# Optimization experiments

Hardware: AMD Instinct MI355X
Metric: run time of the kernel (lower is better)

The kernel has to match this reference:

```python
import jax, jax.numpy as jnp
import numpy as np
from jax import lax

B, T, K = 4096, 512, 7


def setup_inputs() -> dict:
    key = jax.random.key(0)
    k1, k2, k3, k4, k5, k6 = jax.random.split(key, 6)
    emissions = jax.random.normal(k1, (B, T, K), dtype=jnp.float32)
    # variable-length sequences: mask is a contiguous prefix of ones (token_ids.gt(0))
    lengths = jax.random.randint(k2, (B,), T // 2, T + 1)
    mask = (jnp.arange(T)[None, :] < lengths[:, None]).astype(jnp.int32)
    tags = jax.random.randint(k3, (B, T), 0, K).astype(jnp.int64)
    transitions = jax.random.normal(k4, (K, K), dtype=jnp.float32) * 0.1
    start_transitions = jax.random.normal(k5, (K,), dtype=jnp.float32) * 0.1
    end_transitions = jax.random.normal(k6, (K,), dtype=jnp.float32) * 0.1
    return {
        "emissions": emissions,
        "mask": mask,
        "tags": tags,
        "transitions": transitions,
        "start_transitions": start_transitions,
        "end_transitions": end_transitions,
    }


def _crf_nll(emissions, mask, tags, transitions, start_transitions, end_transitions):
    maskf = mask.astype(emissions.dtype)  # [B, T]
    # ---- numerator: score of the gold path ----
    em_tag = jnp.take_along_axis(emissions, tags[..., None], axis=2)[..., 0]  # [B, T]
    score = start_transitions[tags[:, 0]] + em_tag[:, 0]  # [B]
    trans_score = transitions[tags[:, :-1], tags[:, 1:]]  # [B, T-1]
    score = score + jnp.sum((trans_score + em_tag[:, 1:]) * maskf[:, 1:], axis=1)
    last_idx = jnp.sum(mask, axis=1).astype(jnp.int32) - 1  # [B]
    last_tag = jnp.take_along_axis(tags, last_idx[:, None].astype(tags.dtype), axis=1)[:, 0]
    score = score + end_transitions[last_tag]
    # ---- denominator: log partition via forward algorithm (stable logsumexp DP) ----
    alpha0 = start_transitions[None, :] + emissions[:, 0]  # [B, K]

    def step(alpha, xs):
        em_t, m_t = xs  # [B, K], [B]
        # alpha[b, i] + transitions[i, j] + em_t[b, j] -> logsumexp over i
        nxt = jax.nn.logsumexp(alpha[:, :, None] + transitions[None, :, :] + em_t[:, None, :], axis=1)
        alpha = jnp.where(m_t[:, None] > 0, nxt, alpha)
        return alpha, None

    xs = (jnp.swapaxes(emissions[:, 1:], 0, 1), jnp.swapaxes(mask[:, 1:], 0, 1))  # [T-1, B, K], [T-1, B]
    alpha, _ = lax.scan(step, alpha0, xs)
    log_z = jax.nn.logsumexp(alpha + end_transitions[None, :], axis=1)  # [B]
    return jnp.mean(log_z - score)


def reference(emissions, mask, tags, transitions, start_transitions, end_transitions):
    return _crf_nll(emissions, mask, tags, transitions, start_transitions, end_transitions)
```

## Files before the change

### kernel.cpp

```cpp
#include <hip/hip_runtime.h>

#define BB 4096
#define TT 512
#define KK 7
#define SS 16
#define NMAT (BB * 31 * 7)

__device__ __forceinline__ float fexp2(float x){ float r; asm("v_exp_f32 %0, %1" : "=v"(r) : "v"(x)); return r; }
__device__ __forceinline__ float flog2(float x){ float r; asm("v_log_f32 %0, %1" : "=v"(r) : "v"(x)); return r; }
__device__ __forceinline__ float uni(float x){ return __int_as_float(__builtin_amdgcn_readfirstlane(__float_as_int(x))); }

__global__ __launch_bounds__(256) void crf_p1(
    const float* __restrict__ em, const int* __restrict__ msk,
    const float* __restrict__ trn, const float* __restrict__ stt,
    float* __restrict__ wsA, float* __restrict__ wsP)
{
  const float L2E = 1.44269504088896340736f;
  int tid = blockIdx.x * 256 + threadIdx.x;

  float e2[49];
  #pragma unroll
  for (int i = 0; i < 49; i++) e2[i] = uni(fexp2(trn[i] * L2E));

  if (tid < NMAT) {
    int q = tid / 7, i = tid - q * 7;
    int b = q / 31, c = q - b * 31 + 1;
    int t0 = c * SS;
    const size_t eb = (size_t)b * (TT * KK);

    float R[KK];
    #pragma unroll
    for (int j = 0; j < KK; j++) R[j] = (j == i) ? 1.f : 0.f;
    float Lr = 0.f; int cnt = 0; int alive = 1;

    for (int g = 0; g < 4; g++) {
      if (!alive) break;
      int t = t0 + 4 * g;
      float em_[28];
      #pragma unroll
      for (int p = 0; p < 7; p++) {
        float4 f = *(const float4*)(em + eb + (size_t)t * KK + 4 * p);
        em_[4*p+0] = f.x; em_[4*p+1] = f.y; em_[4*p+2] = f.z; em_[4*p+3] = f.w;
      }
      int4 m4 = *(const int4*)(msk + b * TT + t);
      int ms[4] = {m4.x, m4.y, m4.z, m4.w};
      #pragma unroll
      for (int s = 0; s < 4; s++) {
        if (!ms[s]) { alive = 0; break; }
        cnt++;
        float acc[KK];
        #pragma unroll
        for (int j = 0; j < KK; j++) acc[j] = R[0] * e2[j];
        #pragma unroll
        for (int k = 1; k < KK; k++)
          #pragma unroll
          for (int j = 0; j < KK; j++) acc[j] = fmaf(R[k], e2[k*KK + j], acc[j]);
        #pragma unroll
        for (int j = 0; j < KK; j++) R[j] = acc[j] * fexp2(em_[s*KK + j] * L2E);
        if ((cnt & 3) == 0) {
          float mm = R[0];
          #pragma unroll
          for (int j = 1; j < KK; j++) mm = fmaxf(mm, R[j]);
          int ex = (int)((__float_as_uint(mm) >> 23) & 255) - 127;
          float scl = __uint_as_float((unsigned)(127 - ex) << 23);
          Lr += (float)ex;
          #pragma unroll
          for (int j = 0; j < KK; j++) R[j] *= scl;
        }
      }
    }
    if (cnt > 0) {
      float* P = wsP + ((size_t)(c - 1) * BB + b) * 49 + i * KK;
      #pragma unroll
      for (int j = 0; j < KK; j++) P[j] = Lr + flog2(R[j]);
    }
  } else {
    int b = tid - NMAT;
    const size_t eb = (size_t)b * (TT * KK);
    float em_[28];
    #pragma unroll
    for (int p = 0; p < 7; p++) {
      float4 f = *(const float4*)(em + eb + 4 * p);
      em_[4*p+0] = f.x; em_[4*p+1] = f.y; em_[4*p+2] = f.z; em_[4*p+3] = f.w;
    }
    int4 m4 = *(const int4*)(msk + b * TT);
    int ms[4] = {m4.x, m4.y, m4.z, m4.w};

    float u[KK], Ls;
    {
      float a2[KK];
      #pragma unroll
      for (int j = 0; j < KK; j++) a2[j] = (stt[j] + em_[j]) * L2E;
      float m = a2[0];
      #pragma unroll
      for (int j = 1; j < KK; j++) m = fmaxf(m, a2[j]);
      #pragma unroll
      for (int j = 0; j < KK; j++) u[j] = fexp2(a2[j] - m);
      Ls = m;
    }
    int cnt = ms[0]; int alive = 1;

    for (int g = 0; g < 4; g++) {
      if (g > 0) {
        if (!alive) break;
        int t = 4 * g;
        #pragma unroll
        for (int p = 0; p < 7; p++) {
          float4 f = *(const float4*)(em + eb + (size_t)t * KK + 4 * p);
          em_[4*p+0] = f.x; em_[4*p+1] = f.y; em_[4*p+2] = f.z; em_[4*p+3] = f.w;
        }
        int4 n4 = *(const int4*)(msk + b * TT + t);
        ms[0] = n4.x; ms[1] = n4.y; ms[2] = n4.z; ms[3] = n4.w;
      }
      #pragma unroll
      for (int s = 0; s < 4; s++) {
        if (g == 0 && s == 0) continue;
        if (!ms[s]) { alive = 0; break; }
        cnt++;
        float acc[KK];
        #pragma unroll
        for (int j = 0; j < KK; j++) acc[j] = u[0] * e2[j];
        #pragma unroll
        for (int k = 1; k < KK; k++)
          #pragma unroll
          for (int j = 0; j < KK; j++) acc[j] = fmaf(u[k], e2[k*KK + j], acc[j]);
        #pragma unroll
        for (int j = 0; j < KK; j++) u[j] = acc[j] * fexp2(em_[s*KK + j] * L2E);
        if ((cnt & 3) == 0) {
          float mm = u[0];
          #pragma unroll
          for (int j = 1; j < KK; j++) mm = fmaxf(mm, u[j]);
          int ex = (int)((__float_as_uint(mm) >> 23) & 255) - 127;
          float scl = __uint_as_float((unsigned)(127 - ex) << 23);
          Ls += (float)ex;
          #pragma unroll
          for (int j = 0; j < KK; j++) u[j] *= scl;
        }
      }
    }
    #pragma unroll
    for (int j = 0; j < KK; j++) wsA[b * 8 + j] = Ls + flog2(u[j]);
  }
}

__global__ __launch_bounds__(256) void crf_p2(
    const float* __restrict__ em, const int* __restrict__ msk,
    const int* __restrict__ tgs, const float* __restrict__ trn,
    const float* __restrict__ stt, const float* __restrict__ ent,
    const float* __restrict__ wsA, const float* __restrict__ wsP,
    float* __restrict__ out)
{
  const float L2E = 1.44269504088896340736f;
  const float LN2 = 0.69314718055994530942f;
  __shared__ float sm[4];
  int w = threadIdx.x >> 6, lane = threadIdx.x & 63;
  int b = blockIdx.x * 4 + w;
  const int* mrow = msk + b * TT;
  const int* trow = tgs + b * TT;
  const size_t eb = (size_t)b * (TT * KK);

  int4 ma = *(const int4*)(mrow + lane * 8);
  int4 mb = *(const int4*)(mrow + lane * 8 + 4);
  int len = ma.x + ma.y + ma.z + ma.w + mb.x + mb.y + mb.z + mb.w;
  #pragma unroll
  for (int o = 1; o < 64; o <<= 1) len += __shfl_xor(len, o);

  int4 ta = *(const int4*)(trow + lane * 8);
  int4 tb = *(const int4*)(trow + lane * 8 + 4);
  int tga[8] = {ta.x, ta.y, ta.z, ta.w, tb.x, tb.y, tb.z, tb.w};
  int tprev = lane ? trow[lane * 8 - 1] : 0;
  float scp = 0.f;
  #pragma unroll
  for (int s = 0; s < 8; s++) {
    int t = lane * 8 + s; int tg = tga[s];
    if (t == 0)          scp += stt[tg] + em[eb + tg];
    else if (t < len)    scp += trn[tprev * KK + tg] + em[eb + (size_t)t * KK + tg];
    if (t == len - 1)    scp += ent[tg];
    tprev = tg;
  }
  float score = scp;
  #pragma unroll
  for (int o = 1; o < 64; o <<= 1) score += __shfl_xor(score, o);

  float A = (lane < KK) ? wsA[b * 8 + lane] : -1e30f;
  int j = (lane < KK) ? lane : 0;
  int nact = (len - 1) >> 4; if (nact > 31) nact = 31;
  const float* Pb = wsP + (size_t)b * 49;
  const size_t cs = (size_t)BB * 49;
  float cur[KK];
  if (nact >= 1) {
    #pragma unroll
    for (int i = 0; i < KK; i++) cur[i] = Pb[i * KK + j];
  }
  for (int c2 = 1; c2 <= nact; c2++) {
    float nxt[KK];
    if (c2 < nact) {
      #pragma unroll
      for (int i = 0; i < KK; i++) nxt[i] = Pb[(size_t)c2 * cs + i * KK + j];
    }
    float v[KK];
    #pragma unroll
    for (int i = 0; i < KK; i++) v[i] = __shfl(A, i) + cur[i];
    float m = v[0];
    #pragma unroll
    for (int i = 1; i < KK; i++) m = fmaxf(m, v[i]);
    float ssum = 0.f;
    #pragma unroll
    for (int i = 0; i < KK; i++) ssum += fexp2(v[i] - m);
    A = m + flog2(ssum);
    #pragma unroll
    for (int i = 0; i < KK; i++) cur[i] = nxt[i];
  }

  float x = (lane < KK) ? A + ent[lane] * L2E : -1e30f;
  float mx = x;
  #pragma unroll
  for (int o = 1; o < 8; o <<= 1) mx = fmaxf(mx, __shfl_xor(mx, o));
  float se = fexp2(x - mx);
  #pragma unroll
  for (int o = 1; o < 8; o <<= 1) se += __shfl_xor(se, o);

  if (lane == 0) {
    float logz = LN2 * (mx + flog2(se));
    sm[w] = (logz - score) * (1.0f / BB);
  }
  __syncthreads();
  if (threadIdx.x == 0) atomicAdd(out, sm[0] + sm[1] + sm[2] + sm[3]);
}

extern "C" void kernel_launch(void* const* d_in, const int* in_sizes, int n_in,
                              void* d_out, int out_size, void* d_ws, size_t ws_size,
                              hipStream_t stream) {
  const float* em  = (const float*)d_in[0];
  const int*   msk = (const int*)d_in[1];
  const int*   tgs = (const int*)d_in[2];
  const float* trn = (const float*)d_in[3];
  const float* stt = (const float*)d_in[4];
  const float* ent = (const float*)d_in[5];
  float* out = (float*)d_out;

  float* wsA = (float*)d_ws;
  float* wsP = wsA + (size_t)BB * 8;

  hipMemsetAsync(out, 0, sizeof(float), stream);
  hipLaunchKernelGGL(crf_p1, dim3((NMAT + BB) / 256), dim3(256), 0, stream,
                     em, msk, trn, stt, wsA, wsP);
  hipLaunchKernelGGL(crf_p2, dim3(BB / 4), dim3(256), 0, stream,
                     em, msk, tgs, trn, stt, ent, wsA, wsP, out);
}
```

Measured before the change: 179.7 us.

## Precompute sequence lengths and exp transitions in a prepass; double-buffer emission loads

Adds a small prepass kernel that computes each sequence's length from the mask and the exponentiated transition matrix once. The chunk kernel then reads the length instead of per-step mask loads, skips fully masked chunks up front, and double-buffers emission loads so the next group is fetched while the current one is computed. Thread-to-chunk mapping is changed so consecutive threads cover different batch rows within the same chunk. The cost is an extra kernel launch and extra workspace, plus a change in memory access pattern.

```diff
diff --git a/kernel.cpp b/kernel.cpp
--- a/kernel.cpp
+++ b/kernel.cpp
@@ -10,9 +10,64 @@
 __device__ __forceinline__ float flog2(float x){ float r; asm("v_log_f32 %0, %1" : "=v"(r) : "v"(x)); return r; }
 __device__ __forceinline__ float uni(float x){ return __int_as_float(__builtin_amdgcn_readfirstlane(__float_as_int(x))); }
 
+__global__ __launch_bounds__(256) void crf_len(
+    const int* __restrict__ msk, const float* __restrict__ trn,
+    int* __restrict__ wlen, float* __restrict__ wse2)
+{
+  const float L2E = 1.44269504088896340736f;
+  if (blockIdx.x == 0 && threadIdx.x < 49)
+    wse2[threadIdx.x] = fexp2(trn[threadIdx.x] * L2E);
+  int gid = blockIdx.x * 256 + threadIdx.x;
+  int b = gid >> 6, lane = gid & 63;
+  int4 a = *(const int4*)(msk + b * TT + lane * 8);
+  int4 c = *(const int4*)(msk + b * TT + lane * 8 + 4);
+  int s = a.x + a.y + a.z + a.w + c.x + c.y + c.z + c.w;
+  #pragma unroll
+  for (int o = 1; o < 64; o <<= 1) s += __shfl_xor(s, o);
+  if (lane == 0) wlen[b] = s;
+}
+
+__device__ __forceinline__ void loadg(float* B, const float* ep, int g){
+  #pragma unroll
+  for (int p = 0; p < 7; p++){
+    float4 f = *(const float4*)(ep + g * 28 + 4 * p);
+    B[4*p] = f.x; B[4*p+1] = f.y; B[4*p+2] = f.z; B[4*p+3] = f.w;
+  }
+}
+
+template<int S0>
+__device__ __forceinline__ void step4(float* R, float& Lr, const float* E,
+                                      int base, int a, const float* e2){
+  const float L2E = 1.44269504088896340736f;
+  #pragma unroll
+  for (int s = S0; s < 4; s++){
+    if (base + s < a){
+      float acc[KK];
+      #pragma unroll
+      for (int j = 0; j < KK; j++) acc[j] = R[0] * e2[j];
+      #pragma unroll
+      for (int k = 1; k < KK; k++)
+        #pragma unroll
+        for (int j = 0; j < KK; j++) acc[j] = fmaf(R[k], e2[k*KK + j], acc[j]);
+      #pragma unroll
+      for (int j = 0; j < KK; j++) R[j] = acc[j] * fexp2(E[s*KK + j] * L2E);
+    }
+  }
+  if (base + 3 < a){
+    float mm = R[0];
+    #pragma unroll
+    for (int j = 1; j < KK; j++) mm = fmaxf(mm, R[j]);
+    int ex = (int)((__float_as_uint(mm) >> 23) & 255) - 127;
+    float scl = __uint_as_float((unsigned)(127 - ex) << 23);
+    Lr += (float)ex;
+    #pragma unroll
+    for (int j = 0; j < KK; j++) R[j] *= scl;
+  }
+}
+
 __global__ __launch_bounds__(256) void crf_p1(
-    const float* __restrict__ em, const int* __restrict__ msk,
-    const float* __restrict__ trn, const float* __restrict__ stt,
+    const float* __restrict__ em, const int* __restrict__ wlen,
+    const float* __restrict__ wse2, const float* __restrict__ stt,
     float* __restrict__ wsA, float* __restrict__ wsP)
 {
   const float L2E = 1.44269504088896340736f;
@@ -20,77 +75,50 @@
 
   float e2[49];
   #pragma unroll
-  for (int i = 0; i < 49; i++) e2[i] = uni(fexp2(trn[i] * L2E));
+  for (int i = 0; i < 49; i++) e2[i] = uni(wse2[i]);
 
   if (tid < NMAT) {
     int q = tid / 7, i = tid - q * 7;
-    int b = q / 31, c = q - b * 31 + 1;
+    int c = (q >> 12) + 1, b = q & (BB - 1);
     int t0 = c * SS;
-    const size_t eb = (size_t)b * (TT * KK);
-
-    float R[KK];
-    #pragma unroll
-    for (int j = 0; j < KK; j++) R[j] = (j == i) ? 1.f : 0.f;
-    float Lr = 0.f; int cnt = 0; int alive = 1;
-
-    for (int g = 0; g < 4; g++) {
-      if (!alive) break;
-      int t = t0 + 4 * g;
-      float em_[28];
-      #pragma unroll
-      for (int p = 0; p < 7; p++) {
-        float4 f = *(const float4*)(em + eb + (size_t)t * KK + 4 * p);
-        em_[4*p+0] = f.x; em_[4*p+1] = f.y; em_[4*p+2] = f.z; em_[4*p+3] = f.w;
-      }
-      int4 m4 = *(const int4*)(msk + b * TT + t);
-      int ms[4] = {m4.x, m4.y, m4.z, m4.w};
-      #pragma unroll
-      for (int s = 0; s < 4; s++) {
-        if (!ms[s]) { alive = 0; break; }
-        cnt++;
-        float acc[KK];
-        #pragma unroll
-        for (int j = 0; j < KK; j++) acc[j] = R[0] * e2[j];
-        #pragma unroll
-        for (int k = 1; k < KK; k++)
-          #pragma unroll
-          for (int j = 0; j < KK; j++) acc[j] = fmaf(R[k], e2[k*KK + j], acc[j]);
-        #pragma unroll
-        for (int j = 0; j < KK; j++) R[j] = acc[j] * fexp2(em_[s*KK + j] * L2E);
-        if ((cnt & 3) == 0) {
-          float mm = R[0];
-          #pragma unroll
-          for (int j = 1; j < KK; j++) mm = fmaxf(mm, R[j]);
-          int ex = (int)((__float_as_uint(mm) >> 23) & 255) - 127;
-          float scl = __uint_as_float((unsigned)(127 - ex) << 23);
-          Lr += (float)ex;
-          #pragma unroll
-          for (int j = 0; j < KK; j++) R[j] *= scl;
+    int len = wlen[b];
+    int a = len - t0; a = a > 16 ? 16 : a;
+    if (a > 0) {
+      const float* ep = em + (size_t)b * (TT * KK) + (size_t)t0 * KK;
+      float R[KK];
+      #pragma unroll
+      for (int j = 0; j < KK; j++) R[j] = (j == i) ? 1.f : 0.f;
+      float Lr = 0.f;
+      float bufA[28], bufB[28];
+      loadg(bufA, ep, 0);
+      if (a > 4) loadg(bufB, ep, 1);
+      step4<0>(R, Lr, bufA, 0, a, e2);
+      if (a > 4) {
+        if (a > 8) loadg(bufA, ep, 2);
+        step4<0>(R, Lr, bufB, 4, a, e2);
+        if (a > 8) {
+          if (a > 12) loadg(bufB, ep, 3);
+          step4<0>(R, Lr, bufA, 8, a, e2);
+          if (a > 12) step4<0>(R, Lr, bufB, 12, a, e2);
         }
       }
-    }
-    if (cnt > 0) {
       float* P = wsP + ((size_t)(c - 1) * BB + b) * 49 + i * KK;
       #pragma unroll
       for (int j = 0; j < KK; j++) P[j] = Lr + flog2(R[j]);
     }
   } else {
     int b = tid - NMAT;
-    const size_t eb = (size_t)b * (TT * KK);
-    float em_[28];
-    #pragma unroll
-    for (int p = 0; p < 7; p++) {
-      float4 f = *(const float4*)(em + eb + 4 * p);
-      em_[4*p+0] = f.x; em_[4*p+1] = f.y; em_[4*p+2] = f.z; em_[4*p+3] = f.w;
-    }
-    int4 m4 = *(const int4*)(msk + b * TT);
-    int ms[4] = {m4.x, m4.y, m4.z, m4.w};
-
+    int len = wlen[b];
+    int a = len > 16 ? 16 : len;
+    const float* ep = em + (size_t)b * (TT * KK);
+    float bufA[28], bufB[28];
+    loadg(bufA, ep, 0);
+    if (a > 4) loadg(bufB, ep, 1);
     float u[KK], Ls;
     {
       float a2[KK];
       #pragma unroll
-      for (int j = 0; j < KK; j++) a2[j] = (stt[j] + em_[j]) * L2E;
+      for (int j = 0; j < KK; j++) a2[j] = (stt[j] + bufA[j]) * L2E;
       float m = a2[0];
       #pragma unroll
       for (int j = 1; j < KK; j++) m = fmaxf(m, a2[j]);
@@ -98,45 +126,15 @@
       for (int j = 0; j < KK; j++) u[j] = fexp2(a2[j] - m);
       Ls = m;
     }
-    int cnt = ms[0]; int alive = 1;
-
-    for (int g = 0; g < 4; g++) {
-      if (g > 0) {
-        if (!alive) break;
-        int t = 4 * g;
-        #pragma unroll
-        for (int p = 0; p < 7; p++) {
-          float4 f = *(const float4*)(em + eb + (size_t)t * KK + 4 * p);
-          em_[4*p+0] = f.x; em_[4*p+1] = f.y; em_[4*p+2] = f.z; em_[4*p+3] = f.w;
-        }
-        int4 n4 = *(const int4*)(msk + b * TT + t);
-        ms[0] = n4.x; ms[1] = n4.y; ms[2] = n4.z; ms[3] = n4.w;
+    step4<1>(u, Ls, bufA, 0, a, e2);
+    if (a > 4) {
+      if (a > 8) loadg(bufA, ep, 2);
+      step4<0>(u, Ls, bufB, 4, a, e2);
+      if (a > 8) {
+        if (a > 12) loadg(bufB, ep, 3);
+        step4<0>(u, Ls, bufA, 8, a, e2);
+        if (a > 12) step4<0>(u, Ls, bufB, 12, a, e2);
       }
-      #pragma unroll
-      for (int s = 0; s < 4; s++) {
-        if (g == 0 && s == 0) continue;
-        if (!ms[s]) { alive = 0; break; }
-        cnt++;
-        float acc[KK];
-        #pragma unroll
-        for (int j = 0; j < KK; j++) acc[j] = u[0] * e2[j];
-        #pragma unroll
-        for (int k = 1; k < KK; k++)
-          #pragma unroll
-          for (int j = 0; j < KK; j++) acc[j] = fmaf(u[k], e2[k*KK + j], acc[j]);
-        #pragma unroll
-        for (int j = 0; j < KK; j++) u[j] = acc[j] * fexp2(em_[s*KK + j] * L2E);
-        if ((cnt & 3) == 0) {
-          float mm = u[0];
-          #pragma unroll
-          for (int j = 1; j < KK; j++) mm = fmaxf(mm, u[j]);
-          int ex = (int)((__float_as_uint(mm) >> 23) & 255) - 127;
-          float scl = __uint_as_float((unsigned)(127 - ex) << 23);
-          Ls += (float)ex;
-          #pragma unroll
-          for (int j = 0; j < KK; j++) u[j] *= scl;
-        }
-      }
     }
     #pragma unroll
     for (int j = 0; j < KK; j++) wsA[b * 8 + j] = Ls + flog2(u[j]);
@@ -144,10 +142,10 @@
 }
 
 __global__ __launch_bounds__(256) void crf_p2(
-    const float* __restrict__ em, const int* __restrict__ msk,
-    const int* __restrict__ tgs, const float* __restrict__ trn,
-    const float* __restrict__ stt, const float* __restrict__ ent,
-    const float* __restrict__ wsA, const float* __restrict__ wsP,
+    const float* __restrict__ em, const int* __restrict__ tgs,
+    const float* __restrict__ trn, const float* __restrict__ stt,
+    const float* __restrict__ ent, const float* __restrict__ wsA,
+    const float* __restrict__ wsP, const int* __restrict__ wlen,
     float* __restrict__ out)
 {
   const float L2E = 1.44269504088896340736f;
@@ -155,15 +153,9 @@
   __shared__ float sm[4];
   int w = threadIdx.x >> 6, lane = threadIdx.x & 63;
   int b = blockIdx.x * 4 + w;
-  const int* mrow = msk + b * TT;
   const int* trow = tgs + b * TT;
   const size_t eb = (size_t)b * (TT * KK);
-
-  int4 ma = *(const int4*)(mrow + lane * 8);
-  int4 mb = *(const int4*)(mrow + lane * 8 + 4);
-  int len = ma.x + ma.y + ma.z + ma.w + mb.x + mb.y + mb.z + mb.w;
-  #pragma unroll
-  for (int o = 1; o < 64; o <<= 1) len += __shfl_xor(len, o);
+  int len = wlen[b];
 
   int4 ta = *(const int4*)(trow + lane * 8);
   int4 tb = *(const int4*)(trow + lane * 8 + 4);
@@ -239,12 +231,16 @@
   const float* ent = (const float*)d_in[5];
   float* out = (float*)d_out;
 
-  float* wsA = (float*)d_ws;
-  float* wsP = wsA + (size_t)BB * 8;
+  float* wsA  = (float*)d_ws;
+  float* wsP  = wsA + (size_t)BB * 8;
+  float* wse2 = wsP + (size_t)31 * BB * 49;
+  int*   wlen = (int*)(wse2 + 64);
 
   hipMemsetAsync(out, 0, sizeof(float), stream);
+  hipLaunchKernelGGL(crf_len, dim3(BB * 64 / 256), dim3(256), 0, stream,
+                     msk, trn, wlen, wse2);
   hipLaunchKernelGGL(crf_p1, dim3((NMAT + BB) / 256), dim3(256), 0, stream,
-                     em, msk, trn, stt, wsA, wsP);
+                     em, wlen, wse2, stt, wsA, wsP);
   hipLaunchKernelGGL(crf_p2, dim3(BB / 4), dim3(256), 0, stream,
-                     em, msk, tgs, trn, stt, ent, wsA, wsP, out);
-}
+                     em, tgs, trn, stt, ent, wsA, wsP, wlen, out);
+}
```

New measurement: 167.4 us. 1.07x faster.
